# Performance work log

Hardware: AMD Instinct MI355X
Metric: run time of the kernel (lower is better)

## Reference

```python
import jax, jax.numpy as jnp
import numpy as np
import math

B, S, D, H = 4, 1024, 1024, 16
DK = D // H
K_INDEX = 5


def setup_inputs() -> dict:
    key = jax.random.key(0)
    ks = jax.random.split(key, 10)
    s = 0.02
    return {
        "query": jax.random.normal(ks[0], (B, S, D), jnp.float32),
        "key": jax.random.normal(ks[1], (B, S, D), jnp.float32),
        "values": jax.random.normal(ks[2], (B, S, D), jnp.float32),
        "lens": jax.random.randint(ks[3], (B,), 0, S),
        "Wq": jax.random.normal(ks[4], (D, D), jnp.float32) * s,  # shared q/k proj (kq_same=True)
        "bq": jnp.zeros((D,), jnp.float32),
        "Wv": jax.random.normal(ks[5], (D, D), jnp.float32) * s,
        "bv": jnp.zeros((D,), jnp.float32),
        "Wo": jax.random.normal(ks[6], (D, D), jnp.float32) * s,
        "bo": jnp.zeros((D,), jnp.float32),
        "gammas": jax.random.normal(ks[7], (H, 1, 1), jnp.float32) * 0.1,
        "ln_w": jnp.ones((D,), jnp.float32),
        "ln_b": jnp.zeros((D,), jnp.float32),
    }


def _split_heads(x):
    b, s, _ = x.shape
    return x.reshape(b, s, H, DK).transpose(0, 2, 1, 3)  # [B,H,S,DK]


def reference(query, key, values, lens, Wq, bq, Wv, bv, Wo, bo, gammas, ln_w, ln_b):
    # causal mask, peek_cur=False -> strict lower triangle; eval mode (no random masking)
    mask = jnp.tril(jnp.ones((S, S), bool), -1)[None, None]  # [1,1,S,S]

    q = _split_heads(query @ Wq.T + bq)
    k = _split_heads(key @ Wq.T + bq)   # kq_same: shared weights
    v = _split_heads(values @ Wv.T + bv)

    scores = jnp.einsum("bhid,bhjd->bhij", q, k) / math.sqrt(DK)
    NEG = jnp.finfo(scores.dtype).min

    # --- distance-decay term (no_grad in torch -> stop_gradient) ---
    s_ = jax.nn.softmax(jnp.where(mask, scores, NEG), axis=-1)
    distcum = jnp.cumsum(s_, axis=-1)
    disttotal = jnp.sum(s_, axis=-1, keepdims=True)
    idx = jnp.arange(S, dtype=scores.dtype)
    pos_effect = jnp.abs(idx[None, :] - idx[:, None])[None, None]  # |j - i|
    dist = jnp.sqrt(jnp.clip((disttotal - distcum) * pos_effect, 0.0, None))
    dist = jax.lax.stop_gradient(dist)

    gam = -jnp.abs(gammas)[None]  # [1,H,1,1]
    total_effect = jnp.clip(jnp.exp(dist * gam), 1e-5, 1e5)
    scores = scores * total_effect

    scores = jnp.where(mask, scores, NEG)
    p = jax.nn.softmax(scores, axis=-1)
    p = jnp.where(mask, p, 0.0)

    # maxout rescale (peek_cur=False)
    scale = jnp.minimum(1.0 / jnp.max(p, axis=-1, keepdims=True), 5.0)
    p = p * scale

    attn = jnp.einsum("bhij,bhjd->bhid", p, v)
    concat = attn.transpose(0, 2, 1, 3).reshape(B, S, D)
    attn_out = concat @ Wo.T + bo

    # k_select sparsification of the (post-softmax, maxout-scaled) scores
    sc_a = p[:, :, :K_INDEX, :]
    sc_b = p[:, :, K_INDEX:, :]
    kth = jax.lax.top_k(sc_b, K_INDEX)[0][..., -1:]  # k-th largest per row
    sc_b = jnp.where(sc_b >= kth, sc_b, NEG)
    sparse_scores = jax.nn.softmax(jnp.concatenate([sc_a, sc_b], axis=2), axis=-1)

    # residual (eval: dropout is identity) + LayerNorm
    y = query + attn_out
    mu = jnp.mean(y, axis=-1, keepdims=True)
    var = jnp.mean((y - mu) ** 2, axis=-1, keepdims=True)
    out = (y - mu) / jnp.sqrt(var + 1e-5) * ln_w + ln_b
    return (out, sparse_scores)
```

## Files before the change

kernel.cpp:

```cpp
#include <hip/hip_runtime.h>
#include <hip/hip_fp16.h>

#define Ssz 1024
#define Dsz 1024
#define Hsz 16
#define DKsz 64
#define Bsz 4
#define NEGI (-1.0e30f)
#define NEGD (-1.0e300)

typedef float f32x4 __attribute__((ext_vector_type(4)));
typedef _Float16 f16x8 __attribute__((ext_vector_type(8)));

__device__ __forceinline__ float wmaxf(float x) {
#pragma unroll
  for (int o = 32; o; o >>= 1) x = fmaxf(x, __shfl_xor(x, o));
  return x;
}
__device__ __forceinline__ float wsumf(float x) {
#pragma unroll
  for (int o = 32; o; o >>= 1) x += __shfl_xor(x, o);
  return x;
}
__device__ __forceinline__ double wmaxd(double x) {
#pragma unroll
  for (int o = 32; o; o >>= 1) x = fmax(x, __shfl_xor(x, o));
  return x;
}
__device__ __forceinline__ double wsumd(double x) {
#pragma unroll
  for (int o = 32; o; o >>= 1) x += __shfl_xor(x, o);
  return x;
}
__device__ __forceinline__ int wmini(int x) {
#pragma unroll
  for (int o = 32; o; o >>= 1) x = min(x, __shfl_xor(x, o));
  return x;
}
__device__ __forceinline__ int sswz(int c) { return c ^ (((c >> 5) & 7) << 2); }
__device__ __forceinline__ int pswz(int c, int r) { return c ^ (r & 7) ^ ((c >> 3) & 7); }

__global__ __launch_bounds__(256) void gemm_qk(
    const float* __restrict__ A, const float* __restrict__ W,
    const float* __restrict__ bias, __half* __restrict__ ohi, __half* __restrict__ olo) {
  const int w = threadIdx.x >> 6, lane = threadIdx.x & 63;
  const int quad = lane >> 4, l16 = lane & 15;
  const int m0 = blockIdx.x * 64 + w * 16;
  const int n0 = blockIdx.y * 64;
  f32x4 acc[4] = {};
  const size_t arow = (size_t)(m0 + l16) * Dsz;
  for (int k0 = 0; k0 < Dsz; k0 += 32) {
    f16x8 ahi, alo;
    {
      const float* ap = A + arow + k0 + quad * 8;
#pragma unroll
      for (int e = 0; e < 8; e++) {
        const float v = ap[e];
        const _Float16 h = (_Float16)v;
        ahi[e] = h;
        alo[e] = (_Float16)(v - (float)h);
      }
    }
#pragma unroll
    for (int t = 0; t < 4; t++) {
      const float* wp = W + (size_t)(n0 + t * 16 + l16) * Dsz + k0 + quad * 8;
      f16x8 whi, wlo;
#pragma unroll
      for (int e = 0; e < 8; e++) {
        const float v = wp[e];
        const _Float16 h = (_Float16)v;
        whi[e] = h;
        wlo[e] = (_Float16)(v - (float)h);
      }
      acc[t] = __builtin_amdgcn_mfma_f32_16x16x32_f16(ahi, whi, acc[t], 0, 0, 0);
      acc[t] = __builtin_amdgcn_mfma_f32_16x16x32_f16(ahi, wlo, acc[t], 0, 0, 0);
      acc[t] = __builtin_amdgcn_mfma_f32_16x16x32_f16(alo, whi, acc[t], 0, 0, 0);
    }
  }
#pragma unroll
  for (int t = 0; t < 4; t++) {
    const int oc = n0 + t * 16 + l16;
    const float bv = bias[oc];
    const int hh = oc >> 6, dk = oc & 63;
#pragma unroll
    for (int r = 0; r < 4; r++) {
      const int mr = m0 + quad * 4 + r;
      const int bb = mr >> 10, ss = mr & 1023;
      const float v = acc[t][r] + bv;
      const size_t idx = ((size_t)(bb * Hsz + hh) * Ssz + ss) * DKsz + dk;
      const __half h = __float2half(v);
      ohi[idx] = h;
      olo[idx] = __float2half(v - __half2float(h));
    }
  }
}

__global__ __launch_bounds__(256) void gemm_v(
    const float* __restrict__ A, const float* __restrict__ W,
    const float* __restrict__ bias, __half* __restrict__ out_t) {
  const int w = threadIdx.x >> 6, lane = threadIdx.x & 63;
  const int quad = lane >> 4, l16 = lane & 15;
  const int m0 = blockIdx.x * 64 + w * 16;
  const int n0 = blockIdx.y * 64;
  f32x4 acc[4] = {};
  const size_t arow = (size_t)(m0 + l16) * Dsz;
  for (int k0 = 0; k0 < Dsz; k0 += 32) {
    f16x8 ahi;
    {
      const float* ap = A + arow + k0 + quad * 8;
#pragma unroll
      for (int e = 0; e < 8; e++) ahi[e] = (_Float16)ap[e];
    }
#pragma unroll
    for (int t = 0; t < 4; t++) {
      const float* wp = W + (size_t)(n0 + t * 16 + l16) * Dsz + k0 + quad * 8;
      f16x8 whi;
#pragma unroll
      for (int e = 0; e < 8; e++) whi[e] = (_Float16)wp[e];
      acc[t] = __builtin_amdgcn_mfma_f32_16x16x32_f16(ahi, whi, acc[t], 0, 0, 0);
    }
  }
#pragma unroll
  for (int t = 0; t < 4; t++) {
    const int oc = n0 + t * 16 + l16;
    const float bv = bias[oc];
    const int hh = oc >> 6, dk = oc & 63;
#pragma unroll
    for (int r = 0; r < 4; r++) {
      const int mr = m0 + quad * 4 + r;
      const int bb = mr >> 10, ss = mr & 1023;
      out_t[((size_t)(bb * Hsz + hh) * DKsz + dk) * Ssz + ss] = __float2half(acc[t][r] + bv);
    }
  }
}

__global__ __launch_bounds__(256) void gemm_o(
    const __half* __restrict__ A, const float* __restrict__ W,
    const float* __restrict__ bias, float* __restrict__ outf) {
  const int w = threadIdx.x >> 6, lane = threadIdx.x & 63;
  const int quad = lane >> 4, l16 = lane & 15;
  const int m0 = blockIdx.x * 64 + w * 16;
  const int n0 = blockIdx.y * 64;
  f32x4 acc[4] = {};
  const size_t arow = (size_t)(m0 + l16) * Dsz;
  for (int k0 = 0; k0 < Dsz; k0 += 32) {
    const f16x8 a = *(const f16x8*)(A + arow + k0 + quad * 8);
#pragma unroll
    for (int t = 0; t < 4; t++) {
      const float* wp = W + (size_t)(n0 + t * 16 + l16) * Dsz + k0 + quad * 8;
      f16x8 whi;
#pragma unroll
      for (int e = 0; e < 8; e++) whi[e] = (_Float16)wp[e];
      acc[t] = __builtin_amdgcn_mfma_f32_16x16x32_f16(a, whi, acc[t], 0, 0, 0);
    }
  }
#pragma unroll
  for (int t = 0; t < 4; t++) {
    const int oc = n0 + t * 16 + l16;
    const float bv = bias[oc];
#pragma unroll
    for (int r = 0; r < 4; r++) {
      const int mr = m0 + quad * 4 + r;
      outf[(size_t)mr * Dsz + oc] = acc[t][r] + bv;
    }
  }
}


__global__ __launch_bounds__(256) void attn_scores(
    const __half* __restrict__ qhi, const __half* __restrict__ qlo,
    const __half* __restrict__ khi, const __half* __restrict__ klo,
    float* __restrict__ scores, int bh0) {
  const int w = threadIdx.x >> 6, lane = threadIdx.x & 63;
  const int quad = lane >> 4, l16 = lane & 15;
  const int lbh = blockIdx.y, bh = bh0 + lbh;
  for (int cc = 0; cc < 2; cc++) {
    const int chunk = cc ? (63 - (int)blockIdx.x) : (int)blockIdx.x;
    const int i0 = chunk * 16;
    const size_t qb = ((size_t)bh * Ssz + i0 + l16) * DKsz + quad * 8;
    const f16x8 ah0 = *(const f16x8*)(qhi + qb);
    const f16x8 ah1 = *(const f16x8*)(qhi + qb + 32);
    const f16x8 al0 = *(const f16x8*)(qlo + qb);
    const f16x8 al1 = *(const f16x8*)(qlo + qb + 32);
    float* dst = scores + ((size_t)lbh * Ssz + i0) * Ssz;
    for (int tt = 0; tt < 16; tt++) {
      const int n0 = (w + tt * 4) * 16;
      if (n0 > i0 + 14) continue;
      const size_t kb = ((size_t)bh * Ssz + n0 + l16) * DKsz + quad * 8;
      const f16x8 bh0v = *(const f16x8*)(khi + kb);
      const f16x8 bh1v = *(const f16x8*)(khi + kb + 32);
      const f16x8 bl0v = *(const f16x8*)(klo + kb);
      const f16x8 bl1v = *(const f16x8*)(klo + kb + 32);
      f32x4 accs = {};
      accs = __builtin_amdgcn_mfma_f32_16x16x32_f16(al0, bl0v, accs, 0, 0, 0);
      accs = __builtin_amdgcn_mfma_f32_16x16x32_f16(al1, bl1v, accs, 0, 0, 0);
      accs = __builtin_amdgcn_mfma_f32_16x16x32_f16(ah0, bl0v, accs, 0, 0, 0);
      accs = __builtin_amdgcn_mfma_f32_16x16x32_f16(ah1, bl1v, accs, 0, 0, 0);
      accs = __builtin_amdgcn_mfma_f32_16x16x32_f16(al0, bh0v, accs, 0, 0, 0);
      accs = __builtin_amdgcn_mfma_f32_16x16x32_f16(al1, bh1v, accs, 0, 0, 0);
      accs = __builtin_amdgcn_mfma_f32_16x16x32_f16(ah0, bh0v, accs, 0, 0, 0);
      accs = __builtin_amdgcn_mfma_f32_16x16x32_f16(ah1, bh1v, accs, 0, 0, 0);
#pragma unroll
      for (int r = 0; r < 4; r++)
        dst[(size_t)(quad * 4 + r) * Ssz + n0 + l16] = accs[r] * 0.125f;
    }
  }
}

__global__ __launch_bounds__(256) void attn_soft(
    float* __restrict__ scores, const float* __restrict__ gam,
    float* __restrict__ sparse, int bh0) {
  const int w = threadIdx.x >> 6, lane = threadIdx.x & 63;
  const int lbh = blockIdx.y, bh = bh0 + lbh;
  const int hidx = bh & 15;
  const float gf = -fabsf(gam[hidx]);
  for (int cc = 0; cc < 2; cc++) {
    const int chunk = cc ? (63 - (int)blockIdx.x) : (int)blockIdx.x;
    const int i0 = chunk * 16;
    for (int rr = 0; rr < 4; rr++) {
      const int gi = i0 + w * 4 + rr;
      const int nch = __builtin_amdgcn_readfirstlane((gi + 63) >> 6);
      float* rowp = scores + ((size_t)lbh * Ssz + gi) * Ssz;
      float xf[16];
      float m1 = NEGI;
#pragma unroll
      for (int e = 0; e < 16; e++) {
        if (e < nch) {
          const int j = 64 * e + lane;
          xf[e] = rowp[j];
          if (j < gi) m1 = fmaxf(m1, xf[e]);
        }
      }
      m1 = wmaxf(m1);
      float s[16];
      float ls = 0.f;
#pragma unroll
      for (int e = 0; e < 16; e++) {
        s[e] = 0.f;
        if (e < nch) {
          const int j = 64 * e + lane;
          const float v = (j < gi) ? __expf(xf[e] - m1) : 0.f;
          s[e] = v;
          ls += v;
        }
      }
      ls = wsumf(ls);
      const float invls = (ls > 0.f) ? 1.0f / ls : 0.f;
      float tot[16];
#pragma unroll
      for (int e = 0; e < 16; e++) {
        if (e < nch) {
          const float q = s[e] * invls;
          float v = __shfl_down(q, 1);
          if (lane == 63) v = 0.f;
#pragma unroll
          for (int o = 1; o < 64; o <<= 1) {
            const float t = __shfl_down(v, o);
            if (lane + o < 64) v += t;
          }
          s[e] = v;
          tot[e] = __shfl(q + v, 0);
        }
      }
      {
        float csum = 0.f;
#pragma unroll
        for (int e = 15; e >= 0; e--) {
          if (e < nch) {
            s[e] = s[e] + csum;
            csum += tot[e];
          }
        }
      }
      float ys[16];
      float m2 = NEGI;
#pragma unroll
      for (int e = 0; e < 16; e++) {
        ys[e] = NEGI;
        if (e < nch) {
          const int j = 64 * e + lane;
          if (j < gi) {
            const float pe = (float)(gi - j);
            const float tl = s[e] > 0.f ? s[e] * pe : 0.f;
            float te = __expf(gf * sqrtf(tl));
            te = te < 1e-5f ? 1e-5f : te;
            const float vv = xf[e] * te;
            ys[e] = vv;
            m2 = fmaxf(m2, vv);
          }
        }
      }
      m2 = wmaxf(m2);
      float xs[16];
      float ls3 = 0.f;
#pragma unroll
      for (int e = 0; e < 16; e++) {
        xs[e] = 0.f;
        if (e < nch) {
          const int j = 64 * e + lane;
          const float ev = (j < gi) ? __expf(ys[e] - m2) : 0.f;
          xs[e] = ev;
          ls3 += ev;
        }
      }
      ls3 = wsumf(ls3);
      const float inv2 = (ls3 > 0.f) ? 1.0f / ls3 : 0.f;
      float mp = 0.f;
#pragma unroll
      for (int e = 0; e < 16; e++) {
        xs[e] *= inv2;
        mp = fmaxf(mp, xs[e]);
      }
      mp = wmaxf(mp);
      const float scl = (mp > 0.f) ? fminf(1.0f / mp, 5.0f) : 5.0f;
#pragma unroll
      for (int e = 0; e < 16; e++) xs[e] *= scl;
      {
        _Float16* prow = (_Float16*)rowp;
#pragma unroll
        for (int e = 0; e < 16; e++) prow[64 * e + lane] = (_Float16)xs[e];
      }
      float m3 = 0.f;
#pragma unroll
      for (int e = 0; e < 16; e++) m3 = fmaxf(m3, xs[e]);
      m3 = wmaxf(m3);

      float* dst = sparse + ((size_t)bh * Ssz + gi) * Ssz;
      if (gi < 5) {
        float o4[16];
        float ls4 = 0.f;
#pragma unroll
        for (int e = 0; e < 16; e++) {
          const float ev = expf(xs[e] - m3);
          o4[e] = ev;
          ls4 += ev;
        }
        const float inv3 = 1.0f / fmaxf(wsumf(ls4), 1e-30f);
#pragma unroll
        for (int e = 0; e < 16; e++) dst[64 * e + lane] = o4[e] * inv3;
      } else {
        float m5 = 0.f, m6 = 0.f;
        {
          unsigned int removed = 0;
          for (int r6 = 0; r6 < 6; r6++) {
            float lm = NEGI;
#pragma unroll
            for (int e = 0; e < 16; e++)
              if (!((removed >> e) & 1)) lm = fmaxf(lm, ys[e]);
            const float m = wmaxf(lm);
            int li = 1 << 30;
#pragma unroll
            for (int e = 0; e < 16; e++)
              if (!((removed >> e) & 1) && ys[e] == m) li = min(li, 64 * e + lane);
            li = wmini(li);
            if ((li & 63) == lane) removed |= 1u << (li >> 6);
            if (r6 == 4) m5 = m;
            if (r6 == 5) m6 = m;
          }
        }
        const float bstar = 0.5f * (m5 + m6);
        const float ETA = 6e-5f;
        const float wlo = m6 - 0.1f, whi = m5 + 0.1f;
        float md[16];
        float mn = 0.f;
#pragma unroll
        for (int e = 0; e < 16; e++) {
          md[e] = 0.f;
          if (e < nch) {
            const int j = 64 * e + lane;
            if (j < gi && ys[e] >= wlo && ys[e] <= whi) {
              const float pe = (float)(gi - j);
              const float t0 = fmaxf(s[e], 0.f);
              float telo = __expf(gf * sqrtf(fmaxf(t0 - ETA, 0.f) * pe));
              telo = fminf(fmaxf(telo, 1e-5f), 1.0f);
              float tehi = __expf(gf * sqrtf((t0 + ETA) * pe));
              tehi = fminf(fmaxf(tehi, 1e-5f), 1.0f);
              md[e] = fminf(fabsf(xf[e]) * (telo - tehi) + 2e-4f, 0.04f);
              mn = fmaxf(mn, md[e]);
            }
          }
        }
        mn = wmaxf(mn);
        float cK = 0.f, cA = 0.f;
        unsigned int mK = 0, mA = 0;
#pragma unroll
        for (int e = 0; e < 16; e++) {
          if (e < nch) {
            const int j = 64 * e + lane;
            if (j < gi) {
              const float margin = fminf(1.5f * (md[e] + mn) + 1e-4f, 0.06f);
              if (ys[e] > bstar + margin) {
                mK |= 1u << e; cK += 1.f;
              } else if (!(ys[e] < bstar - margin)) {
                mA |= 1u << e; cA += 1.f;
              }
            }
          }
        }
        float vvf[16];
        float vK = 0.f, vA = 0.f;
#pragma unroll
        for (int e = 0; e < 16; e++) {
          vvf[e] = 0.f;
          if (((mK | mA) >> e) & 1) {
            const float val = __expf(xs[e] - m3);
            vvf[e] = val;
            if ((mK >> e) & 1) vK += val; else vA += val;
          }
        }
        vK = wsumf(vK); vA = wsumf(vA);
        cK = wsumf(cK); cA = wsumf(cA);
        const float vbar = (cA > 0.5f) ? vA / cA : 0.f;
        const float Zhat = vK + (5.0f - cK) * vbar;
        const float invZ = (Zhat > 0.f) ? 1.0f / Zhat : 0.f;
#pragma unroll
        for (int e = 0; e < 16; e++) {
          const bool isK = (mK >> e) & 1;
          const bool isA = (mA >> e) & 1;
          const float o = isK ? vvf[e] * invZ : isA ? 0.5f * vvf[e] * invZ : 0.f;
          dst[64 * e + lane] = o;
        }
      }
    }
  }
}

__global__ __launch_bounds__(256) void attn_pv(
    const float* __restrict__ scoresP, const __half* __restrict__ vt,
    __half* __restrict__ attn_c, int bh0) {
  const int w = threadIdx.x >> 6, lane = threadIdx.x & 63;
  const int quad = lane >> 4, l16 = lane & 15;
  const int lbh = blockIdx.y, bh = bh0 + lbh;
  const int hidx = bh & 15, bidx = bh >> 4;
  const _Float16* pb = (const _Float16*)scoresP;
  const int dk0 = w * 16;
  for (int cc = 0; cc < 2; cc++) {
    const int chunk = cc ? (63 - (int)blockIdx.x) : (int)blockIdx.x;
    const int i0 = chunk * 16;
    const int kmax = (i0 + 15 + 31) & ~31;
    f32x4 acc = {};
    const size_t prow = ((size_t)lbh * Ssz + i0 + l16) * 2048;
    const size_t vrow = ((size_t)bh * DKsz + dk0 + l16) * Ssz;
    for (int k0 = 0; k0 < kmax; k0 += 32) {
      const f16x8 a = *(const f16x8*)(pb + prow + k0 + quad * 8);
      const f16x8 b = *(const f16x8*)(vt + vrow + k0 + quad * 8);
      acc = __builtin_amdgcn_mfma_f32_16x16x32_f16(a, b, acc, 0, 0, 0);
    }
#pragma unroll
    for (int r = 0; r < 4; r++) {
      const int ss = i0 + quad * 4 + r;
      attn_c[((size_t)bidx * Ssz + ss) * Dsz + hidx * DKsz + dk0 + l16] = __float2half(acc[r]);
    }
  }
}

__global__ __launch_bounds__(256) void attn_kernel(
    const __half* __restrict__ qhi, const __half* __restrict__ qlo,
    const __half* __restrict__ khi, const __half* __restrict__ klo,
    const __half* __restrict__ vt, const float* __restrict__ gam,
    __half* __restrict__ attn_c, float* __restrict__ sparse) {
  __shared__ __align__(16) float sc[16 * 1024];
  const int w = threadIdx.x >> 6, lane = threadIdx.x & 63;
  const int quad = lane >> 4, l16 = lane & 15;
  const int bh = blockIdx.y, i0 = blockIdx.x * 16;
  const int hidx = bh & 15, bidx = bh >> 4;
  _Float16* pbase = (_Float16*)sc;

  {
    const size_t qb = ((size_t)bh * Ssz + i0 + l16) * DKsz + quad * 8;
    const f16x8 ah0 = *(const f16x8*)(qhi + qb);
    const f16x8 ah1 = *(const f16x8*)(qhi + qb + 32);
    const f16x8 al0 = *(const f16x8*)(qlo + qb);
    const f16x8 al1 = *(const f16x8*)(qlo + qb + 32);
    for (int tt = 0; tt < 16; tt++) {
      const int n0 = (w + tt * 4) * 16;
      const size_t kb = ((size_t)bh * Ssz + n0 + l16) * DKsz + quad * 8;
      const f16x8 bh0 = *(const f16x8*)(khi + kb);
      const f16x8 bh1 = *(const f16x8*)(khi + kb + 32);
      const f16x8 bl0 = *(const f16x8*)(klo + kb);
      const f16x8 bl1 = *(const f16x8*)(klo + kb + 32);
      f32x4 accs = {};
      accs = __builtin_amdgcn_mfma_f32_16x16x32_f16(al0, bl0, accs, 0, 0, 0);
      accs = __builtin_amdgcn_mfma_f32_16x16x32_f16(al1, bl1, accs, 0, 0, 0);
      accs = __builtin_amdgcn_mfma_f32_16x16x32_f16(ah0, bl0, accs, 0, 0, 0);
      accs = __builtin_amdgcn_mfma_f32_16x16x32_f16(ah1, bl1, accs, 0, 0, 0);
      accs = __builtin_amdgcn_mfma_f32_16x16x32_f16(al0, bh0, accs, 0, 0, 0);
      accs = __builtin_amdgcn_mfma_f32_16x16x32_f16(al1, bh1, accs, 0, 0, 0);
      accs = __builtin_amdgcn_mfma_f32_16x16x32_f16(ah0, bh0, accs, 0, 0, 0);
      accs = __builtin_amdgcn_mfma_f32_16x16x32_f16(ah1, bh1, accs, 0, 0, 0);
      const int pc = sswz(n0 + l16);
#pragma unroll
      for (int r = 0; r < 4; r++)
        sc[(quad * 4 + r) * 1024 + pc] = accs[r] * 0.125f;
    }
  }
  __syncthreads();

  {
    const double g = -fabs((double)gam[hidx]);
    for (int rr = 0; rr < 4; rr++) {
      const int r = w * 4 + rr, gi = i0 + r;
      float xf[16];
#pragma unroll
      for (int q4 = 0; q4 < 4; q4++) {
        const f32x4 t = *(const f32x4*)(sc + r * 1024 + sswz(lane * 16 + q4 * 4));
#pragma unroll
        for (int e = 0; e < 4; e++) xf[q4 * 4 + e] = t[e];
      }
      float m1 = NEGI;
#pragma unroll
      for (int e = 0; e < 16; e++) {
        const int j = lane * 16 + e;
        if (j < gi) m1 = fmaxf(m1, xf[e]);
      }
      m1 = wmaxf(m1);
      double s[16];
      double ls = 0.0;
#pragma unroll
      for (int e = 0; e < 16; e++) {
        const int j = lane * 16 + e;
        const double v = (j < gi) ? exp((double)xf[e] - (double)m1) : 0.0;
        s[e] = v;
        ls += v;
      }
      ls = wsumd(ls);
      const double invls = (ls > 0.0) ? 1.0 / ls : 0.0;
      double lt = 0.0;
#pragma unroll
      for (int e = 0; e < 16; e++) { s[e] *= invls; lt += s[e]; }
      double v = __shfl_down(lt, 1);
      if (lane == 63) v = 0.0;
#pragma unroll
      for (int o = 1; o < 64; o <<= 1) {
        const double t = __shfl_down(v, o);
        if (lane + o < 64) v += t;
      }
      double run = v;
#pragma unroll
      for (int e = 15; e >= 0; e--) {
        const double tmp = s[e];
        s[e] = run;
        run += tmp;
      }
      double ys[16], xs[16];
      double m2 = NEGD;
#pragma unroll
      for (int e = 0; e < 16; e++) {
        const int j = lane * 16 + e;
        if (j < gi) {
          const double pe = (double)(gi - j);
          const double tl = s[e] > 0.0 ? s[e] * pe : 0.0;
          double te = exp(g * sqrt(tl));
          te = te < 1e-5 ? 1e-5 : te;
          const double vv = (double)xf[e] * te;
          ys[e] = vv;
          m2 = fmax(m2, vv);
        } else {
          ys[e] = NEGD;
        }
      }
      m2 = wmaxd(m2);
      double ls3 = 0.0;
#pragma unroll
      for (int e = 0; e < 16; e++) {
        const int j = lane * 16 + e;
        const double ev = (j < gi) ? exp(ys[e] - m2) : 0.0;
        xs[e] = ev;
        ls3 += ev;
      }
      ls3 = wsumd(ls3);
      const double inv2 = (ls3 > 0.0) ? 1.0 / ls3 : 0.0;
      double mp = 0.0;
#pragma unroll
      for (int e = 0; e < 16; e++) {
        xs[e] *= inv2;
        mp = fmax(mp, xs[e]);
      }
      mp = wmaxd(mp);
      const double scl = (mp > 0.0) ? fmin(1.0 / mp, 5.0) : 5.0;
#pragma unroll
      for (int e = 0; e < 16; e++) xs[e] *= scl;
      {
        __align__(16) _Float16 hb[16];
#pragma unroll
        for (int e = 0; e < 16; e++) hb[e] = (_Float16)(float)xs[e];
        const int c0 = lane * 2;
        *(f16x8*)(pbase + r * 2048 + pswz(c0, r) * 8) = *(const f16x8*)&hb[0];
        *(f16x8*)(pbase + r * 2048 + pswz(c0 + 1, r) * 8) = *(const f16x8*)&hb[8];
      }
      double m3 = 0.0;
#pragma unroll
      for (int e = 0; e < 16; e++) m3 = fmax(m3, xs[e]);
      m3 = wmaxd(m3);

      float* dst = sparse + ((size_t)bh * Ssz + gi) * Ssz + lane * 16;
      if (gi < 5) {
        float o4[16];
        float ls4 = 0.f;
#pragma unroll
        for (int e = 0; e < 16; e++) {
          const float ev = expf((float)(xs[e] - m3));
          o4[e] = ev;
          ls4 += ev;
        }
        const float inv3 = 1.0f / fmaxf(wsumf(ls4), 1e-30f);
#pragma unroll
        for (int q4 = 0; q4 < 4; q4++) {
          f32x4 st;
#pragma unroll
          for (int e = 0; e < 4; e++) st[e] = o4[q4 * 4 + e] * inv3;
          *(f32x4*)(dst + q4 * 4) = st;
        }
      } else {
        double m5 = 0.0, m6 = 0.0;
        {
          unsigned int removed = 0;
          for (int r6 = 0; r6 < 6; r6++) {
            double lm = NEGD;
#pragma unroll
            for (int e = 0; e < 16; e++)
              if (!((removed >> e) & 1)) lm = fmax(lm, ys[e]);
            const double m = wmaxd(lm);
            int li = 1 << 30;
#pragma unroll
            for (int e = 0; e < 16; e++)
              if (!((removed >> e) & 1) && ys[e] == m) li = min(li, lane * 16 + e);
            li = wmini(li);
            if ((li >> 4) == lane) removed |= 1u << (li & 15);
            if (r6 == 4) m5 = m;
            if (r6 == 5) m6 = m;
          }
        }
        const double bstar = 0.5 * (m5 + m6);
        const double ETA = 6e-5;
        double md[16];
#pragma unroll
        for (int e = 0; e < 16; e++) {
          const int j = lane * 16 + e;
          if (j < gi) {
            const double pe = (double)(gi - j);
            const double t0 = fmax(s[e], 0.0);
            double telo = exp(g * sqrt(fmax(t0 - ETA, 0.0) * pe));
            telo = fmin(fmax(telo, 1e-5), 1.0);
            double tehi = exp(g * sqrt((t0 + ETA) * pe));
            tehi = fmin(fmax(tehi, 1e-5), 1.0);
            md[e] = fmin(fabs((double)xf[e]) * (telo - tehi) + 2e-4, 0.04);
          } else {
            md[e] = 0.0;
          }
        }
        double mn = 0.0;
#pragma unroll
        for (int e = 0; e < 16; e++) {
          const int j = lane * 16 + e;
          if (j < gi && ys[e] >= m6 - 0.1 && ys[e] <= m5 + 0.1) mn = fmax(mn, md[e]);
        }
        mn = wmaxd(mn);
        double vK = 0.0, vA = 0.0, cK = 0.0, cA = 0.0;
        double vv[16];
        int cls[16];
#pragma unroll
        for (int e = 0; e < 16; e++) {
          const int j = lane * 16 + e;
          if (j < gi) {
            const double margin = fmin(1.5 * (md[e] + mn) + 1e-4, 0.06);
            const double val = exp(xs[e] - m3);
            vv[e] = val;
            if (ys[e] > bstar + margin) {
              cls[e] = 2; vK += val; cK += 1.0;
            } else if (ys[e] < bstar - margin) {
              cls[e] = 0;
            } else {
              cls[e] = 1; vA += val; cA += 1.0;
            }
          } else {
            cls[e] = 0;
            vv[e] = 0.0;
          }
        }
        vK = wsumd(vK); vA = wsumd(vA);
        cK = wsumd(cK); cA = wsumd(cA);
        const double vbar = (cA > 0.5) ? vA / cA : 0.0;
        const double Zhat = vK + (5.0 - cK) * vbar;
        const double invZ = (Zhat > 0.0) ? 1.0 / Zhat : 0.0;
#pragma unroll
        for (int q4 = 0; q4 < 4; q4++) {
          f32x4 st;
#pragma unroll
          for (int e4 = 0; e4 < 4; e4++) {
            const int e = q4 * 4 + e4;
            const double o =
                (cls[e] == 2) ? vv[e] * invZ : (cls[e] == 1) ? 0.5 * vv[e] * invZ : 0.0;
            st[e4] = (float)o;
          }
          *(f32x4*)(dst + q4 * 4) = st;
        }
      }
    }
  }
  __syncthreads();

  {
    const int dk0 = w * 16;
    f32x4 acc = {};
    for (int k0 = 0; k0 < Ssz; k0 += 32) {
      const int cch = (k0 >> 3) + quad;
      const f16x8 a = *(const f16x8*)(pbase + l16 * 2048 + pswz(cch, l16) * 8);
      const f16x8 b =
          *(const f16x8*)(vt + ((size_t)bh * DKsz + dk0 + l16) * Ssz + k0 + quad * 8);
      acc = __builtin_amdgcn_mfma_f32_16x16x32_f16(a, b, acc, 0, 0, 0);
    }
#pragma unroll
    for (int r = 0; r < 4; r++) {
      const int ss = i0 + quad * 4 + r;
      attn_c[((size_t)bidx * Ssz + ss) * Dsz + hidx * DKsz + dk0 + l16] = __float2half(acc[r]);
    }
  }
}

__global__ __launch_bounds__(256) void ln_kernel(
    const float* __restrict__ query, const float* __restrict__ attn_out,
    const float* __restrict__ ln_w, const float* __restrict__ ln_b,
    float* __restrict__ out) {
  __shared__ float red[8];
  const int n = blockIdx.x, t = threadIdx.x;
  const int w = t >> 6, lane = t & 63;
  float y[4];
  float s = 0.f, s2 = 0.f;
#pragma unroll
  for (int k = 0; k < 4; k++) {
    const int j = t + k * 256;
    const float v = query[(size_t)n * Dsz + j] + attn_out[(size_t)n * Dsz + j];
    y[k] = v;
    s += v;
    s2 += v * v;
  }
  s = wsumf(s);
  s2 = wsumf(s2);
  if (lane == 0) { red[w] = s; red[4 + w] = s2; }
  __syncthreads();
  s = red[0] + red[1] + red[2] + red[3];
  s2 = red[4] + red[5] + red[6] + red[7];
  const float mu = s * (1.0f / 1024.0f);
  const float var = fmaxf(s2 * (1.0f / 1024.0f) - mu * mu, 0.0f);
  const float rs = rsqrtf(var + 1e-5f);
#pragma unroll
  for (int k = 0; k < 4; k++) {
    const int j = t + k * 256;
    out[(size_t)n * Dsz + j] = (y[k] - mu) * rs * ln_w[j] + ln_b[j];
  }
}

extern "C" void kernel_launch(void* const* d_in, const int* in_sizes, int n_in,
                              void* d_out, int out_size, void* d_ws, size_t ws_size,
                              hipStream_t stream) {
  (void)in_sizes; (void)n_in; (void)out_size;
  const float* query = (const float*)d_in[0];
  const float* key = (const float*)d_in[1];
  const float* values = (const float*)d_in[2];
  const float* Wq = (const float*)d_in[4];
  const float* bq = (const float*)d_in[5];
  const float* Wv = (const float*)d_in[6];
  const float* bv = (const float*)d_in[7];
  const float* Wo = (const float*)d_in[8];
  const float* bo = (const float*)d_in[9];
  const float* gam = (const float*)d_in[10];
  const float* lnw = (const float*)d_in[11];
  const float* lnb = (const float*)d_in[12];

  char* ws = (char*)d_ws;
  const size_t MB = 1024u * 1024u;
  const size_t MB8 = 8u * MB;
  __half* qhi = (__half*)ws;
  __half* qlo = (__half*)(ws + 1 * MB8);
  __half* khi = (__half*)(ws + 2 * MB8);
  __half* klo = (__half*)(ws + 3 * MB8);
  __half* vt = (__half*)(ws + 4 * MB8);
  __half* attn_c = (__half*)(ws + 5 * MB8);
  float* attn_out = (float*)ws;
  float* scores = (float*)(ws + 6 * MB8);

  float* out = (float*)d_out;
  float* sparse = out + (size_t)Bsz * Ssz * Dsz;

  const size_t avail = (ws_size > 6 * MB8) ? (ws_size - 6 * MB8) : 0;
  int cbh = 0;
  if (avail >= 64u * 4u * MB) cbh = 64;
  else if (avail >= 32u * 4u * MB) cbh = 32;
  else if (avail >= 16u * 4u * MB) cbh = 16;
  else if (avail >= 8u * 4u * MB) cbh = 8;

  const dim3 gg(64, 16), gb(256);
  gemm_qk<<<gg, gb, 0, stream>>>(query, Wq, bq, qhi, qlo);
  gemm_qk<<<gg, gb, 0, stream>>>(key, Wq, bq, khi, klo);
  gemm_v<<<gg, gb, 0, stream>>>(values, Wv, bv, vt);
  if (cbh > 0) {
    for (int bh0 = 0; bh0 < Bsz * Hsz; bh0 += cbh) {
      attn_scores<<<dim3(32, cbh), 256, 0, stream>>>(qhi, qlo, khi, klo, scores, bh0);
      attn_soft<<<dim3(32, cbh), 256, 0, stream>>>(scores, gam, sparse, bh0);
      attn_pv<<<dim3(32, cbh), 256, 0, stream>>>(scores, vt, attn_c, bh0);
    }
  } else {
    attn_kernel<<<dim3(64, 64), 256, 0, stream>>>(qhi, qlo, khi, klo, vt, gam, attn_c, sparse);
  }
  gemm_o<<<gg, gb, 0, stream>>>(attn_c, Wo, bo, attn_out);
  ln_kernel<<<(Bsz * Ssz), 256, 0, stream>>>(query, attn_out, lnw, lnb, out);
}
```

Before: 1.499 ms.

## Pre-split weights to fp16 once and streamline softmax and top-k reductions

Adds small kernels that convert Wq, Wv and Wo to fp16 hi/lo halves once per call. The GEMMs then load packed fp16 weights with vector loads instead of converting fp32 weights element by element in every block. In the softmax kernel, the post-softmax max is derived from the pre-normalization max, which removes two cross-lane reductions. The top-k argmax now uses a ballot instead of a min reduction, and the two counts are packed into one reduction. Costs are two extra launches and workspace aliasing with buffers, which is only safe if they are dead at that point.

```diff
diff --git a/kernel.cpp b/kernel.cpp
--- a/kernel.cpp
+++ b/kernel.cpp
@@ -11,6 +11,7 @@
 
 typedef float f32x4 __attribute__((ext_vector_type(4)));
 typedef _Float16 f16x8 __attribute__((ext_vector_type(8)));
+typedef _Float16 f16x4 __attribute__((ext_vector_type(4)));
 
 __device__ __forceinline__ float wmaxf(float x) {
 #pragma unroll
@@ -40,9 +41,39 @@
 __device__ __forceinline__ int sswz(int c) { return c ^ (((c >> 5) & 7) << 2); }
 __device__ __forceinline__ int pswz(int c, int r) { return c ^ (r & 7) ^ ((c >> 3) & 7); }
 
+__global__ __launch_bounds__(256) void wsplit_qv(
+    const float* __restrict__ Wq, const float* __restrict__ Wv,
+    __half* __restrict__ wqhi, __half* __restrict__ wqlo, __half* __restrict__ wvhi) {
+  const size_t i = ((size_t)blockIdx.x * 256 + threadIdx.x) * 4;
+  const f32x4 q = *(const f32x4*)(Wq + i);
+  const f32x4 v = *(const f32x4*)(Wv + i);
+  f16x4 hq, lq, hv;
+#pragma unroll
+  for (int e = 0; e < 4; e++) {
+    const _Float16 h = (_Float16)q[e];
+    hq[e] = h;
+    lq[e] = (_Float16)(q[e] - (float)h);
+    hv[e] = (_Float16)v[e];
+  }
+  *(f16x4*)((_Float16*)wqhi + i) = hq;
+  *(f16x4*)((_Float16*)wqlo + i) = lq;
+  *(f16x4*)((_Float16*)wvhi + i) = hv;
+}
+
+__global__ __launch_bounds__(256) void wsplit_o(
+    const float* __restrict__ Wo, __half* __restrict__ wohi) {
+  const size_t i = ((size_t)blockIdx.x * 256 + threadIdx.x) * 4;
+  const f32x4 v = *(const f32x4*)(Wo + i);
+  f16x4 hv;
+#pragma unroll
+  for (int e = 0; e < 4; e++) hv[e] = (_Float16)v[e];
+  *(f16x4*)((_Float16*)wohi + i) = hv;
+}
+
 __global__ __launch_bounds__(256) void gemm_qk(
-    const float* __restrict__ A, const float* __restrict__ W,
-    const float* __restrict__ bias, __half* __restrict__ ohi, __half* __restrict__ olo) {
+    const float* __restrict__ A, const __half* __restrict__ wqhi,
+    const __half* __restrict__ wqlo, const float* __restrict__ bias,
+    __half* __restrict__ ohi, __half* __restrict__ olo) {
   const int w = threadIdx.x >> 6, lane = threadIdx.x & 63;
   const int quad = lane >> 4, l16 = lane & 15;
   const int m0 = blockIdx.x * 64 + w * 16;
@@ -63,15 +94,9 @@
     }
 #pragma unroll
     for (int t = 0; t < 4; t++) {
-      const float* wp = W + (size_t)(n0 + t * 16 + l16) * Dsz + k0 + quad * 8;
-      f16x8 whi, wlo;
-#pragma unroll
-      for (int e = 0; e < 8; e++) {
-        const float v = wp[e];
-        const _Float16 h = (_Float16)v;
-        whi[e] = h;
-        wlo[e] = (_Float16)(v - (float)h);
-      }
+      const size_t woff = (size_t)(n0 + t * 16 + l16) * Dsz + k0 + quad * 8;
+      const f16x8 whi = *(const f16x8*)((const _Float16*)wqhi + woff);
+      const f16x8 wlo = *(const f16x8*)((const _Float16*)wqlo + woff);
       acc[t] = __builtin_amdgcn_mfma_f32_16x16x32_f16(ahi, whi, acc[t], 0, 0, 0);
       acc[t] = __builtin_amdgcn_mfma_f32_16x16x32_f16(ahi, wlo, acc[t], 0, 0, 0);
       acc[t] = __builtin_amdgcn_mfma_f32_16x16x32_f16(alo, whi, acc[t], 0, 0, 0);
@@ -96,7 +121,7 @@
 }
 
 __global__ __launch_bounds__(256) void gemm_v(
-    const float* __restrict__ A, const float* __restrict__ W,
+    const float* __restrict__ A, const __half* __restrict__ wvhi,
     const float* __restrict__ bias, __half* __restrict__ out_t) {
   const int w = threadIdx.x >> 6, lane = threadIdx.x & 63;
   const int quad = lane >> 4, l16 = lane & 15;
@@ -113,10 +138,8 @@
     }
 #pragma unroll
     for (int t = 0; t < 4; t++) {
-      const float* wp = W + (size_t)(n0 + t * 16 + l16) * Dsz + k0 + quad * 8;
-      f16x8 whi;
-#pragma unroll
-      for (int e = 0; e < 8; e++) whi[e] = (_Float16)wp[e];
+      const size_t woff = (size_t)(n0 + t * 16 + l16) * Dsz + k0 + quad * 8;
+      const f16x8 whi = *(const f16x8*)((const _Float16*)wvhi + woff);
       acc[t] = __builtin_amdgcn_mfma_f32_16x16x32_f16(ahi, whi, acc[t], 0, 0, 0);
     }
   }
@@ -135,7 +158,7 @@
 }
 
 __global__ __launch_bounds__(256) void gemm_o(
-    const __half* __restrict__ A, const float* __restrict__ W,
+    const __half* __restrict__ A, const __half* __restrict__ wohi,
     const float* __restrict__ bias, float* __restrict__ outf) {
   const int w = threadIdx.x >> 6, lane = threadIdx.x & 63;
   const int quad = lane >> 4, l16 = lane & 15;
@@ -147,10 +170,8 @@
     const f16x8 a = *(const f16x8*)(A + arow + k0 + quad * 8);
 #pragma unroll
     for (int t = 0; t < 4; t++) {
-      const float* wp = W + (size_t)(n0 + t * 16 + l16) * Dsz + k0 + quad * 8;
-      f16x8 whi;
-#pragma unroll
-      for (int e = 0; e < 8; e++) whi[e] = (_Float16)wp[e];
+      const size_t woff = (size_t)(n0 + t * 16 + l16) * Dsz + k0 + quad * 8;
+      const f16x8 whi = *(const f16x8*)((const _Float16*)wohi + woff);
       acc[t] = __builtin_amdgcn_mfma_f32_16x16x32_f16(a, whi, acc[t], 0, 0, 0);
     }
   }
@@ -292,7 +313,7 @@
       }
       m2 = wmaxf(m2);
       float xs[16];
-      float ls3 = 0.f;
+      float ls3 = 0.f, mev = 0.f;
 #pragma unroll
       for (int e = 0; e < 16; e++) {
         xs[e] = 0.f;
@@ -301,29 +322,23 @@
           const float ev = (j < gi) ? __expf(ys[e] - m2) : 0.f;
           xs[e] = ev;
           ls3 += ev;
+          mev = fmaxf(mev, ev);
         }
       }
       ls3 = wsumf(ls3);
+      mev = wmaxf(mev);
       const float inv2 = (ls3 > 0.f) ? 1.0f / ls3 : 0.f;
-      float mp = 0.f;
-#pragma unroll
-      for (int e = 0; e < 16; e++) {
-        xs[e] *= inv2;
-        mp = fmaxf(mp, xs[e]);
-      }
-      mp = wmaxf(mp);
+      const float mp = mev * inv2;
       const float scl = (mp > 0.f) ? fminf(1.0f / mp, 5.0f) : 5.0f;
-#pragma unroll
-      for (int e = 0; e < 16; e++) xs[e] *= scl;
+      const float c2 = inv2 * scl;
+#pragma unroll
+      for (int e = 0; e < 16; e++) xs[e] *= c2;
+      const float m3 = mp * scl;
       {
         _Float16* prow = (_Float16*)rowp;
 #pragma unroll
         for (int e = 0; e < 16; e++) prow[64 * e + lane] = (_Float16)xs[e];
       }
-      float m3 = 0.f;
-#pragma unroll
-      for (int e = 0; e < 16; e++) m3 = fmaxf(m3, xs[e]);
-      m3 = wmaxf(m3);
 
       float* dst = sparse + ((size_t)bh * Ssz + gi) * Ssz;
       if (gi < 5) {
@@ -348,12 +363,13 @@
             for (int e = 0; e < 16; e++)
               if (!((removed >> e) & 1)) lm = fmaxf(lm, ys[e]);
             const float m = wmaxf(lm);
-            int li = 1 << 30;
-#pragma unroll
-            for (int e = 0; e < 16; e++)
-              if (!((removed >> e) & 1) && ys[e] == m) li = min(li, 64 * e + lane);
-            li = wmini(li);
-            if ((li & 63) == lane) removed |= 1u << (li >> 6);
+            const unsigned long long bal = __ballot(lm == m);
+            const int src = __ffsll(bal) - 1;
+            int rem_e = 0;
+#pragma unroll
+            for (int e = 15; e >= 0; e--)
+              if (!((removed >> e) & 1) && ys[e] == m) rem_e = e;
+            if (lane == src) removed |= 1u << rem_e;
             if (r6 == 4) m5 = m;
             if (r6 == 5) m6 = m;
           }
@@ -381,7 +397,7 @@
           }
         }
         mn = wmaxf(mn);
-        float cK = 0.f, cA = 0.f;
+        float cnt = 0.f;
         unsigned int mK = 0, mA = 0;
 #pragma unroll
         for (int e = 0; e < 16; e++) {
@@ -390,13 +406,16 @@
             if (j < gi) {
               const float margin = fminf(1.5f * (md[e] + mn) + 1e-4f, 0.06f);
               if (ys[e] > bstar + margin) {
-                mK |= 1u << e; cK += 1.f;
+                mK |= 1u << e; cnt += 1.f;
               } else if (!(ys[e] < bstar - margin)) {
-                mA |= 1u << e; cA += 1.f;
+                mA |= 1u << e; cnt += 2048.f;
               }
             }
           }
         }
+        cnt = wsumf(cnt);
+        const float cA = floorf(cnt * (1.0f / 2048.0f));
+        const float cK = cnt - 2048.0f * cA;
         float vvf[16];
         float vK = 0.f, vA = 0.f;
 #pragma unroll
@@ -409,7 +428,6 @@
           }
         }
         vK = wsumf(vK); vA = wsumf(vA);
-        cK = wsumf(cK); cA = wsumf(cA);
         const float vbar = (cA > 0.5f) ? vA / cA : 0.f;
         const float Zhat = vK + (5.0f - cK) * vbar;
         const float invZ = (Zhat > 0.f) ? 1.0f / Zhat : 0.f;
@@ -780,6 +798,11 @@
   float* attn_out = (float*)ws;
   float* scores = (float*)(ws + 6 * MB8);
 
+  __half* wqhi = (__half*)(ws + 5 * MB8);
+  __half* wqlo = (__half*)(ws + 5 * MB8 + 2 * MB);
+  __half* wvhi = (__half*)(ws + 5 * MB8 + 4 * MB);
+  __half* wohi = (__half*)(ws + 2 * MB8);
+
   float* out = (float*)d_out;
   float* sparse = out + (size_t)Bsz * Ssz * Dsz;
 
@@ -791,9 +814,10 @@
   else if (avail >= 8u * 4u * MB) cbh = 8;
 
   const dim3 gg(64, 16), gb(256);
-  gemm_qk<<<gg, gb, 0, stream>>>(query, Wq, bq, qhi, qlo);
-  gemm_qk<<<gg, gb, 0, stream>>>(key, Wq, bq, khi, klo);
-  gemm_v<<<gg, gb, 0, stream>>>(values, Wv, bv, vt);
+  wsplit_qv<<<1024, 256, 0, stream>>>(Wq, Wv, wqhi, wqlo, wvhi);
+  gemm_qk<<<gg, gb, 0, stream>>>(query, wqhi, wqlo, bq, qhi, qlo);
+  gemm_qk<<<gg, gb, 0, stream>>>(key, wqhi, wqlo, bq, khi, klo);
+  gemm_v<<<gg, gb, 0, stream>>>(values, wvhi, bv, vt);
   if (cbh > 0) {
     for (int bh0 = 0; bh0 < Bsz * Hsz; bh0 += cbh) {
       attn_scores<<<dim3(32, cbh), 256, 0, stream>>>(qhi, qlo, khi, klo, scores, bh0);
@@ -803,6 +827,7 @@
   } else {
     attn_kernel<<<dim3(64, 64), 256, 0, stream>>>(qhi, qlo, khi, klo, vt, gam, attn_c, sparse);
   }
-  gemm_o<<<gg, gb, 0, stream>>>(attn_c, Wo, bo, attn_out);
+  wsplit_o<<<1024, 256, 0, stream>>>(Wo, wohi);
+  gemm_o<<<gg, gb, 0, stream>>>(attn_c, wohi, bo, attn_out);
   ln_kernel<<<(Bsz * Ssz), 256, 0, stream>>>(query, attn_out, lnw, lnb, out);
 }
```

After: 1.334 ms. 1.12x faster.
